# Kernel optimization log

Measured on AMD Instinct MI355X. Metric: run time of the kernel, lower is better.

## Reference

```python
import jax, jax.numpy as jnp
import numpy as np

B, T, H, K, V, O = 4, 2048, 512, 128, 128, 512


def setup_inputs() -> dict:
    key = jax.random.key(0)
    k0, k1, k2 = jax.random.split(key, 3)
    hidden_state = jax.random.normal(k0, (B, T, H), dtype=jnp.float32)
    cell_state = jnp.zeros((B, K, V), dtype=jnp.float32)
    # fused projection: hidden -> [query K, key K, gate K, value V]
    lim_p = np.sqrt(6.0 / (H + 3 * K + V)).astype(np.float32)  # xavier uniform
    proj_w = jax.random.uniform(k1, (3 * K + V, H), jnp.float32, -lim_p, lim_p)
    proj_b = jnp.zeros((3 * K + V,), jnp.float32)
    lim_o = np.sqrt(6.0 / (2 * V + O)).astype(np.float32)
    out_w = jax.random.uniform(k2, (O, 2 * V), jnp.float32, -lim_o, lim_o)
    out_b = jnp.zeros((O,), jnp.float32)
    return {"hidden_state": hidden_state, "cell_state": cell_state,
            "proj_w": proj_w, "proj_b": proj_b, "out_w": out_w, "out_b": out_b}


def reference(hidden_state, cell_state, proj_w, proj_b, out_w, out_b):
    Bq, Tq, _ = hidden_state.shape
    qkgv = hidden_state @ proj_w.T + proj_b          # (B,T,3K+V)
    query = qkgv[..., :K]
    kgate = jax.nn.sigmoid(qkgv[..., K:2 * K])       # key (sigmoid)
    gate = jax.nn.sigmoid(qkgv[..., 2 * K:3 * K])
    value = jnp.tanh(qkgv[..., 3 * K:])              # (B,T,V)

    def step(C, xs):
        q_t, k_t, g_t, v_t = xs                      # (B,K),(B,K),(B,K),(B,V)
        C = C * g_t[..., None] + k_t[..., None] * v_t[..., None, :]  # (B,K,V)
        o_t = jnp.einsum('bkv,bk->bv', C, q_t)       # C^T q
        return C, o_t

    xs = (query.swapaxes(0, 1), kgate.swapaxes(0, 1),
          gate.swapaxes(0, 1), value.swapaxes(0, 1))
    C_final, ov = jax.lax.scan(step, cell_state, xs)
    ov = ov.swapaxes(0, 1)                           # (B,T,V) output_val per step

    # causal Luong dot attention over the growing bank of past output_vals
    scores = jnp.einsum('btv,bsv->bts', ov, ov)      # (B,T,T)
    causal = jnp.tril(jnp.ones((Tq, Tq), dtype=bool))
    scores = jnp.where(causal, scores, -jnp.inf)
    attn = jax.nn.softmax(scores, axis=-1)
    context = jnp.einsum('bts,bsv->btv', attn, ov)   # (B,T,V)

    outputs = jnp.concatenate([ov, context], axis=-1) @ out_w.T + out_b  # (B,T,O)
    return outputs, C_final
```

## Files before the change

kernel.cpp:

```cpp
#include <hip/hip_runtime.h>
#include <hip/hip_bf16.h>


typedef __attribute__((ext_vector_type(8))) short bf16x8;
typedef __attribute__((ext_vector_type(4))) float f32x4;
typedef __attribute__((ext_vector_type(4))) short short4v;

#define MFMA(a,b,c) __builtin_amdgcn_mfma_f32_16x16x32_bf16(a,b,c,0,0,0)

__device__ __forceinline__ short f2b(float x){
  union { float f; unsigned u; } v; v.f = x;
  unsigned r = v.u + 0x7fffu + ((v.u >> 16) & 1u);
  return (short)(r >> 16);
}
__device__ __forceinline__ float b2f(short h){
  union { unsigned u; float f; } v;
  v.u = ((unsigned)(unsigned short)h) << 16;
  return v.f;
}
__device__ __forceinline__ void split2(float x, short& h, short& l){
  h = f2b(x);
  l = f2b(x - b2f(h));
}

__global__ void k_split(const float* __restrict__ in, short* __restrict__ hi,
                        short* __restrict__ lo, int n){
  int i = (blockIdx.x * blockDim.x + threadIdx.x) * 4;
  if (i < n){
    float4 v = *(const float4*)(in + i);
    short4v h, l;
    short th, tl;
    split2(v.x, th, tl); h.x = th; l.x = tl;
    split2(v.y, th, tl); h.y = th; l.y = tl;
    split2(v.z, th, tl); h.z = th; l.z = tl;
    split2(v.w, th, tl); h.w = th; l.w = tl;
    *(short4v*)(hi + i) = h;
    *(short4v*)(lo + i) = l;
  }
}

__global__ void k_cvt(const float* __restrict__ in, short* __restrict__ out, int n){
  int i = (blockIdx.x * blockDim.x + threadIdx.x) * 4;
  if (i < n){
    float4 v = *(const float4*)(in + i);
    short4v o; o.x = f2b(v.x); o.y = f2b(v.y); o.z = f2b(v.z); o.w = f2b(v.w);
    *(short4v*)(out + i) = o;
  }
}

__global__ __launch_bounds__(256) void k_gemm1(
    const short* __restrict__ Ah, const short* __restrict__ Al,
    const short* __restrict__ Bh, const short* __restrict__ Bl,
    const float* __restrict__ bias,
    float* __restrict__ q_o, float* __restrict__ kg_o,
    float* __restrict__ lg_o, float* __restrict__ vv_o)
{
  const int Kd = 512;
  __shared__ __align__(16) short Ash[128][40], Asl[128][40];
  __shared__ __align__(16) short Bsh[64][40],  Bsl[64][40];
  const int m0 = blockIdx.x * 128, n0 = blockIdx.y * 64;
  const int tid = threadIdx.x, lane = tid & 63, w = tid >> 6;
  const int wr = w >> 1, wc = w & 1;
  const int coll = lane & 15, rq = lane >> 4;
  f32x4 acc[4][2];
#pragma unroll
  for (int i = 0; i < 4; i++)
#pragma unroll
    for (int j = 0; j < 2; j++) acc[i][j] = (f32x4){0.f,0.f,0.f,0.f};

  const int ar = tid >> 1, ac = (tid & 1) * 16;
  const int br = tid >> 2, bc = (tid & 3) * 8;

  for (int k0 = 0; k0 < Kd; k0 += 32){
    __syncthreads();
    { size_t g = (size_t)(m0 + ar) * Kd + k0 + ac;
      *(bf16x8*)&Ash[ar][ac]     = *(const bf16x8*)(Ah + g);
      *(bf16x8*)&Ash[ar][ac + 8] = *(const bf16x8*)(Ah + g + 8);
      *(bf16x8*)&Asl[ar][ac]     = *(const bf16x8*)(Al + g);
      *(bf16x8*)&Asl[ar][ac + 8] = *(const bf16x8*)(Al + g + 8); }
    { size_t g = (size_t)(n0 + br) * Kd + k0 + bc;
      *(bf16x8*)&Bsh[br][bc] = *(const bf16x8*)(Bh + g);
      *(bf16x8*)&Bsl[br][bc] = *(const bf16x8*)(Bl + g); }
    __syncthreads();
    bf16x8 ah[4], al[4], bh[2], bl[2];
#pragma unroll
    for (int mi = 0; mi < 4; mi++){
      ah[mi] = *(const bf16x8*)&Ash[wr*64 + mi*16 + coll][rq*8];
      al[mi] = *(const bf16x8*)&Asl[wr*64 + mi*16 + coll][rq*8];
    }
#pragma unroll
    for (int ni = 0; ni < 2; ni++){
      bh[ni] = *(const bf16x8*)&Bsh[wc*32 + ni*16 + coll][rq*8];
      bl[ni] = *(const bf16x8*)&Bsl[wc*32 + ni*16 + coll][rq*8];
    }
#pragma unroll
    for (int mi = 0; mi < 4; mi++)
#pragma unroll
      for (int ni = 0; ni < 2; ni++){
        acc[mi][ni] = MFMA(ah[mi], bh[ni], acc[mi][ni]);
        acc[mi][ni] = MFMA(ah[mi], bl[ni], acc[mi][ni]);
        acc[mi][ni] = MFMA(al[mi], bh[ni], acc[mi][ni]);
      }
  }
#pragma unroll
  for (int mi = 0; mi < 4; mi++)
#pragma unroll
  for (int ni = 0; ni < 2; ni++){
    int gn = n0 + wc*32 + ni*16 + coll;
    float bsv = bias[gn];
    int sec = gn >> 7, jj = gn & 127;
#pragma unroll
    for (int r = 0; r < 4; r++){
      int gm = m0 + wr*64 + mi*16 + rq*4 + r;
      float v = acc[mi][ni][r] + bsv;
      size_t idx = (size_t)gm * 128 + jj;
      if (sec == 0)      q_o[idx] = v;
      else if (sec == 1) kg_o[idx] = 1.f / (1.f + __expf(-v));
      else if (sec == 2) lg_o[idx] = (v > 0.f) ? -log1pf(__expf(-v)) : (v - log1pf(__expf(v)));
      else               vv_o[idx] = tanhf(v);
    }
  }
}

__global__ __launch_bounds__(128) void k_prep(
  const float* __restrict__ q_f, const float* __restrict__ kg_f,
  const float* __restrict__ lg_f, const float* __restrict__ vv_f,
  short* __restrict__ qth, short* __restrict__ qtl,
  short* __restrict__ kth, short* __restrict__ ktl,
  short* __restrict__ khTh, short* __restrict__ khTl,
  short* __restrict__ vvTh, short* __restrict__ vvTl,
  float* __restrict__ Dend)
{
  const int bc = blockIdx.x;
  const int kx = threadIdx.x;
  const size_t base = ((size_t)(bc >> 6) * 2048 + (size_t)(bc & 63) * 32) * 128 + kx;
  double L[32];
  double Lr = 0.0;
#pragma unroll
  for (int s = 0; s < 32; s++){
    size_t idx = base + (size_t)s * 128;
    Lr += (double)lg_f[idx];
    L[s] = Lr;
    float lam  = __expf((float)Lr);
    float ilam = __expf((float)(-Lr));
    short h, l;
    split2(q_f[idx] * lam, h, l);  qth[idx] = h; qtl[idx] = l;
    split2(kg_f[idx] * ilam, h, l); kth[idx] = h; ktl[idx] = l;
  }
  const double Lend = Lr;
  Dend[(size_t)bc * 128 + kx] = (float)exp(Lend);
  __align__(16) short bufh[32], bufl[32];
#pragma unroll
  for (int s = 0; s < 32; s++){
    size_t idx = base + (size_t)s * 128;
    short h, l;
    split2(kg_f[idx] * __expf((float)(Lend - L[s])), h, l);
    bufh[s] = h; bufl[s] = l;
  }
  { short* dh = khTh + ((size_t)bc * 128 + kx) * 32;
    short* dl = khTl + ((size_t)bc * 128 + kx) * 32;
#pragma unroll
    for (int i = 0; i < 32; i += 8){
      *(bf16x8*)(dh + i) = *(const bf16x8*)(bufh + i);
      *(bf16x8*)(dl + i) = *(const bf16x8*)(bufl + i);
    } }
#pragma unroll
  for (int s = 0; s < 32; s++){
    short h, l;
    split2(vv_f[base + (size_t)s * 128], h, l);
    bufh[s] = h; bufl[s] = l;
  }
  { short* dh = vvTh + ((size_t)bc * 128 + kx) * 32;
    short* dl = vvTl + ((size_t)bc * 128 + kx) * 32;
#pragma unroll
    for (int i = 0; i < 32; i += 8){
      *(bf16x8*)(dh + i) = *(const bf16x8*)(bufh + i);
      *(bf16x8*)(dl + i) = *(const bf16x8*)(bufl + i);
    } }
}

__global__ __launch_bounds__(64) void k_scan(
  const short* __restrict__ khTh, const short* __restrict__ khTl,
  const short* __restrict__ vvTh, const short* __restrict__ vvTl,
  const float* __restrict__ Dend, const float* __restrict__ cell0,
  short* __restrict__ sth, short* __restrict__ stl, float* __restrict__ Cfin)
{
  const int blk = blockIdx.x;
  const int b = blk >> 6, tile = blk & 63;
  const int kt = tile >> 3, vt = tile & 7;
  const int lane = threadIdx.x & 63;
  const int coll = lane & 15, rq = lane >> 4;
  const int kcol = kt*16 + coll;
  const int vrow0 = vt*16 + rq*4;
  const size_t cb0 = (size_t)b * 64;

  f32x4 acc;
#pragma unroll
  for (int r = 0; r < 4; r++)
    acc[r] = cell0[((size_t)b*128 + kcol)*128 + vrow0 + r];

  size_t gv = (cb0*128 + vt*16 + coll)*32 + rq*8;
  size_t gk = (cb0*128 + kt*16 + coll)*32 + rq*8;
  bf16x8 avh = *(const bf16x8*)(vvTh + gv);
  bf16x8 avl = *(const bf16x8*)(vvTl + gv);
  bf16x8 bkh = *(const bf16x8*)(khTh + gk);
  bf16x8 bkl = *(const bf16x8*)(khTl + gk);
  float d = Dend[cb0*128 + kcol];

  for (int ck = 0; ck < 64; ck++){
    const size_t cb = cb0 + ck;
    const size_t cbn = cb0 + (ck < 63 ? ck + 1 : ck);
    size_t ngv = (cbn*128 + vt*16 + coll)*32 + rq*8;
    size_t ngk = (cbn*128 + kt*16 + coll)*32 + rq*8;
    bf16x8 navh = *(const bf16x8*)(vvTh + ngv);
    bf16x8 navl = *(const bf16x8*)(vvTl + ngv);
    bf16x8 nbkh = *(const bf16x8*)(khTh + ngk);
    bf16x8 nbkl = *(const bf16x8*)(khTl + ngk);
    float nd = Dend[cbn*128 + kcol];
    {
      size_t sb = (cb*128 + vrow0)*128 + kcol;
#pragma unroll
      for (int r = 0; r < 4; r++){
        short h, l; split2(acc[r], h, l);
        sth[sb + (size_t)r*128] = h;
        stl[sb + (size_t)r*128] = l;
      }
    }
#pragma unroll
    for (int r = 0; r < 4; r++) acc[r] *= d;
    acc = MFMA(avh, bkh, acc);
    acc = MFMA(avh, bkl, acc);
    acc = MFMA(avl, bkh, acc);
    avh = navh; avl = navl; bkh = nbkh; bkl = nbkl; d = nd;
  }
  *(f32x4*)(Cfin + ((size_t)b*128 + kcol)*128 + vrow0) = acc;
}

__global__ __launch_bounds__(256) void k_chunkout(
  const short* __restrict__ qth, const short* __restrict__ qtl,
  const short* __restrict__ kth, const short* __restrict__ ktl,
  const short* __restrict__ vvTh, const short* __restrict__ vvTl,
  const short* __restrict__ sth, const short* __restrict__ stl,
  short* __restrict__ ovT, short* __restrict__ ovc,
  short* __restrict__ ovqh, short* __restrict__ ovql)
{
  __shared__ __align__(16) short ATh[32][40], ATl[32][40];
  const int bc = blockIdx.x;
  const int b = bc >> 6, ck = bc & 63;
  const int tid = threadIdx.x, lane = tid & 63, w = tid >> 6;
  const int coll = lane & 15, rq = lane >> 4;
  const size_t tbase = (size_t)b * 2048 + (size_t)ck * 32;
  {
    const int si = w >> 1, ti = w & 1;
    f32x4 aA = (f32x4){0.f,0.f,0.f,0.f};
#pragma unroll
    for (int kit = 0; kit < 4; kit++){
      size_t ga = (tbase + si*16 + coll) * 128 + kit*32 + rq*8;
      size_t gb = (tbase + ti*16 + coll) * 128 + kit*32 + rq*8;
      bf16x8 a3h = *(const bf16x8*)(kth + ga), a3l = *(const bf16x8*)(ktl + ga);
      bf16x8 b3h = *(const bf16x8*)(qth + gb), b3l = *(const bf16x8*)(qtl + gb);
      aA = MFMA(a3h, b3h, aA);
      aA = MFMA(a3h, b3l, aA);
      aA = MFMA(a3l, b3h, aA);
    }
#pragma unroll
    for (int r = 0; r < 4; r++){
      int s = si*16 + rq*4 + r, t = ti*16 + coll;
      float val = (s <= t) ? aA[r] : 0.f;
      short h, l; split2(val, h, l);
      ATh[t][s] = h; ATl[t][s] = l;
    }
  }
  __syncthreads();
  const int vb = w * 32;
  f32x4 o[2][2];
#pragma unroll
  for (int vi = 0; vi < 2; vi++)
#pragma unroll
    for (int ti = 0; ti < 2; ti++) o[vi][ti] = (f32x4){0.f,0.f,0.f,0.f};
#pragma unroll
  for (int kit = 0; kit < 4; kit++){
    bf16x8 aCh[2], aCl[2], bqh[2], bql[2];
#pragma unroll
    for (int vi = 0; vi < 2; vi++){
      size_t g = ((size_t)bc * 128 + vb + vi*16 + coll) * 128 + kit*32 + rq*8;
      aCh[vi] = *(const bf16x8*)(sth + g);
      aCl[vi] = *(const bf16x8*)(stl + g);
    }
#pragma unroll
    for (int ti = 0; ti < 2; ti++){
      size_t g = (tbase + ti*16 + coll) * 128 + kit*32 + rq*8;
      bqh[ti] = *(const bf16x8*)(qth + g);
      bql[ti] = *(const bf16x8*)(qtl + g);
    }
#pragma unroll
    for (int vi = 0; vi < 2; vi++)
#pragma unroll
      for (int ti = 0; ti < 2; ti++){
        o[vi][ti] = MFMA(aCh[vi], bqh[ti], o[vi][ti]);
        o[vi][ti] = MFMA(aCh[vi], bql[ti], o[vi][ti]);
        o[vi][ti] = MFMA(aCl[vi], bqh[ti], o[vi][ti]);
      }
  }
  {
    bf16x8 a2h[2], a2l[2], b2h[2], b2l[2];
#pragma unroll
    for (int vi = 0; vi < 2; vi++){
      size_t g = ((size_t)bc * 128 + vb + vi*16 + coll) * 32 + rq*8;
      a2h[vi] = *(const bf16x8*)(vvTh + g);
      a2l[vi] = *(const bf16x8*)(vvTl + g);
    }
#pragma unroll
    for (int ti = 0; ti < 2; ti++){
      b2h[ti] = *(const bf16x8*)&ATh[ti*16 + coll][rq*8];
      b2l[ti] = *(const bf16x8*)&ATl[ti*16 + coll][rq*8];
    }
#pragma unroll
    for (int vi = 0; vi < 2; vi++)
#pragma unroll
      for (int ti = 0; ti < 2; ti++){
        o[vi][ti] = MFMA(a2h[vi], b2h[ti], o[vi][ti]);
        o[vi][ti] = MFMA(a2h[vi], b2l[ti], o[vi][ti]);
        o[vi][ti] = MFMA(a2l[vi], b2h[ti], o[vi][ti]);
      }
  }
#pragma unroll
  for (int vi = 0; vi < 2; vi++)
#pragma unroll
  for (int ti = 0; ti < 2; ti++)
#pragma unroll
  for (int r = 0; r < 4; r++){
    int v = vb + vi*16 + rq*4 + r;
    int tl = ti*16 + coll;
    float val = o[vi][ti][r];
    short h, l; split2(val, h, l);
    ovT[((size_t)b * 128 + v) * 2048 + (size_t)ck * 32 + tl] = h;
    ovc[(tbase + tl) * 256 + v] = h;
    ovqh[(tbase + tl) * 128 + v] = h;
    ovql[(tbase + tl) * 128 + v] = l;
  }
}

__global__ __launch_bounds__(256) void k_attn(
  const short* __restrict__ ovqh, const short* __restrict__ ovql,
  const short* __restrict__ ovT, short* __restrict__ ovc)
{
  __shared__ __align__(16) short P[4][16][40];
  const int blk = blockIdx.x;
  const int b = blk >> 5, qi = blk & 31;
  const int qbase = qi * 64;
  const int tid = threadIdx.x, lane = tid & 63, w = tid >> 6;
  const int coll = lane & 15, rq = lane >> 4;
  const int tw = qbase + w * 16;
  const size_t obase = (size_t)b * 2048;
  bf16x8 qfh[4], qfl[4];
#pragma unroll
  for (int kit = 0; kit < 4; kit++){
    size_t g = (obase + tw + coll) * 128 + kit*32 + rq*8;
    qfh[kit] = *(const bf16x8*)(ovqh + g);
    qfl[kit] = *(const bf16x8*)(ovql + g);
  }
  float m[4], l[4];
  f32x4 oa[8];
#pragma unroll
  for (int r = 0; r < 4; r++){ m[r] = -1e30f; l[r] = 0.f; }
#pragma unroll
  for (int df = 0; df < 8; df++) oa[df] = (f32x4){0.f,0.f,0.f,0.f};
  const int smaxv = tw + 15;
  for (int s0 = 0; s0 <= smaxv; s0 += 32){
    f32x4 sc[2];
#pragma unroll
    for (int sf = 0; sf < 2; sf++){
      f32x4 a = (f32x4){0.f,0.f,0.f,0.f};
#pragma unroll
      for (int kit = 0; kit < 4; kit++){
        size_t g = (obase + s0 + sf*16 + coll) * 128 + kit*32 + rq*8;
        bf16x8 kfh = *(const bf16x8*)(ovqh + g);
        bf16x8 kfl = *(const bf16x8*)(ovql + g);
        a = MFMA(qfh[kit], kfh, a);
        a = MFMA(qfh[kit], kfl, a);
        a = MFMA(qfl[kit], kfh, a);
        a = MFMA(qfl[kit], kfl, a);
      }
      sc[sf] = a;
    }
#pragma unroll
    for (int r = 0; r < 4; r++){
      int trow = tw + rq*4 + r;
      float s0v = (s0 + coll      <= trow) ? sc[0][r] : -1e30f;
      float s1v = (s0 + 16 + coll <= trow) ? sc[1][r] : -1e30f;
      float mx = fmaxf(s0v, s1v);
#pragma unroll
      for (int d = 1; d < 16; d <<= 1) mx = fmaxf(mx, __shfl_xor(mx, d));
      float mn = fmaxf(m[r], mx);
      float scale = __expf(m[r] - mn);
      float p0 = __expf(s0v - mn);
      float p1 = __expf(s1v - mn);
      float rs = p0 + p1;
#pragma unroll
      for (int d = 1; d < 16; d <<= 1) rs += __shfl_xor(rs, d);
      l[r] = l[r] * scale + rs;
      m[r] = mn;
#pragma unroll
      for (int df = 0; df < 8; df++) oa[df][r] *= scale;
      P[w][rq*4 + r][coll]      = f2b(p0);
      P[w][rq*4 + r][16 + coll] = f2b(p1);
    }
    bf16x8 pf = *(const bf16x8*)&P[w][coll][rq*8];
#pragma unroll
    for (int df = 0; df < 8; df++){
      bf16x8 vf = *(const bf16x8*)(ovT + ((size_t)b * 128 + df*16 + coll) * 2048 + s0 + rq*8);
      oa[df] = MFMA(pf, vf, oa[df]);
    }
  }
#pragma unroll
  for (int df = 0; df < 8; df++)
#pragma unroll
    for (int r = 0; r < 4; r++){
      int t = tw + rq*4 + r;
      ovc[(obase + t) * 256 + 128 + df*16 + coll] = f2b(oa[df][r] / l[r]);
    }
}

__global__ __launch_bounds__(256) void k_gemm0(
  const short* __restrict__ A, const short* __restrict__ Bw,
  const float* __restrict__ bias, float* __restrict__ out)
{
  const int Kd = 256, N = 512;
  __shared__ __align__(16) short As[128][40];
  __shared__ __align__(16) short Bs[64][40];
  const int m0 = blockIdx.x * 128, n0 = blockIdx.y * 64;
  const int tid = threadIdx.x, lane = tid & 63, w = tid >> 6;
  const int wr = w >> 1, wc = w & 1;
  const int coll = lane & 15, rq = lane >> 4;
  f32x4 acc[4][2];
#pragma unroll
  for (int i = 0; i < 4; i++)
#pragma unroll
    for (int j = 0; j < 2; j++) acc[i][j] = (f32x4){0.f,0.f,0.f,0.f};
  const int ar = tid >> 1, ac = (tid & 1) * 16;
  const int br = tid >> 2, bc = (tid & 3) * 8;
  for (int k0 = 0; k0 < Kd; k0 += 32){
    __syncthreads();
    { const short* g = A + (size_t)(m0 + ar) * Kd + k0 + ac;
      *(bf16x8*)&As[ar][ac]     = *(const bf16x8*)g;
      *(bf16x8*)&As[ar][ac + 8] = *(const bf16x8*)(g + 8); }
    { const short* g = Bw + (size_t)(n0 + br) * Kd + k0 + bc;
      *(bf16x8*)&Bs[br][bc] = *(const bf16x8*)g; }
    __syncthreads();
    bf16x8 a[4], b[2];
#pragma unroll
    for (int mi = 0; mi < 4; mi++) a[mi] = *(const bf16x8*)&As[wr*64 + mi*16 + coll][rq*8];
#pragma unroll
    for (int ni = 0; ni < 2; ni++) b[ni] = *(const bf16x8*)&Bs[wc*32 + ni*16 + coll][rq*8];
#pragma unroll
    for (int mi = 0; mi < 4; mi++)
#pragma unroll
      for (int ni = 0; ni < 2; ni++) acc[mi][ni] = MFMA(a[mi], b[ni], acc[mi][ni]);
  }
#pragma unroll
  for (int mi = 0; mi < 4; mi++)
#pragma unroll
  for (int ni = 0; ni < 2; ni++){
    int gn = n0 + wc*32 + ni*16 + coll;
    float bsv = bias[gn];
#pragma unroll
    for (int r = 0; r < 4; r++){
      int gm = m0 + wr*64 + mi*16 + rq*4 + r;
      out[(size_t)gm * N + gn] = acc[mi][ni][r] + bsv;
    }
  }
}

extern "C" void kernel_launch(void* const* d_in, const int* in_sizes, int n_in,
                              void* d_out, int out_size, void* d_ws, size_t ws_size,
                              hipStream_t stream){
  const float* hidden = (const float*)d_in[0];
  const float* cell0  = (const float*)d_in[1];
  const float* projw  = (const float*)d_in[2];
  const float* projb  = (const float*)d_in[3];
  const float* outw   = (const float*)d_in[4];
  const float* outb   = (const float*)d_in[5];
  float* out = (float*)d_out;

  char* ws = (char*)d_ws;
  size_t off = 0;
  auto alloc = [&](size_t bytes) -> void* {
    void* p = ws + off;
    off += (bytes + 255) & ~(size_t)255;
    return p;
  };
  short* Xh   = (short*)alloc(8192ULL * 512 * 2);
  short* Xl   = (short*)alloc(8192ULL * 512 * 2);
  short* ovqh = Xh;
  short* ovql = Xh + 1048576;
  short* ovT  = Xh + 2097152;
  short* ovc  = Xh + 3145728;
  float* q_f  = (float*)alloc(8192ULL * 128 * 4);
  float* kg_f = (float*)alloc(8192ULL * 128 * 4);
  float* lg_f = (float*)alloc(8192ULL * 128 * 4);
  float* vv_f = (float*)alloc(8192ULL * 128 * 4);
  short* sth  = (short*)q_f;
  short* stl  = sth + 4194304;
  short* Wh   = (short*)alloc(512ULL * 512 * 2);
  short* Wl   = (short*)alloc(512ULL * 512 * 2);
  short* OWbf = (short*)alloc(512ULL * 256 * 2);
  short* qth  = (short*)alloc(8192ULL * 128 * 2);
  short* qtl  = (short*)alloc(8192ULL * 128 * 2);
  short* kth  = (short*)alloc(8192ULL * 128 * 2);
  short* ktl  = (short*)alloc(8192ULL * 128 * 2);
  short* khTh = (short*)alloc(256ULL * 128 * 32 * 2);
  short* khTl = (short*)alloc(256ULL * 128 * 32 * 2);
  short* vvTh = (short*)alloc(256ULL * 128 * 32 * 2);
  short* vvTl = (short*)alloc(256ULL * 128 * 32 * 2);
  float* Dend = (float*)alloc(256ULL * 128 * 4);

  k_split<<<4096, 256, 0, stream>>>(hidden, Xh, Xl, 8192 * 512);
  k_split<<<256,  256, 0, stream>>>(projw,  Wh, Wl, 512 * 512);
  k_cvt<<<128, 256, 0, stream>>>(outw, OWbf, 512 * 256);

  k_gemm1<<<dim3(64, 8), 256, 0, stream>>>(Xh, Xl, Wh, Wl, projb, q_f, kg_f, lg_f, vv_f);
  k_prep<<<256, 128, 0, stream>>>(q_f, kg_f, lg_f, vv_f,
                                  qth, qtl, kth, ktl, khTh, khTl, vvTh, vvTl, Dend);
  k_scan<<<256, 64, 0, stream>>>(khTh, khTl, vvTh, vvTl, Dend, cell0,
                                 sth, stl, out + 8192ULL * 512);
  k_chunkout<<<256, 256, 0, stream>>>(qth, qtl, kth, ktl, vvTh, vvTl, sth, stl,
                                      ovT, ovc, ovqh, ovql);
  k_attn<<<128, 256, 0, stream>>>(ovqh, ovql, ovT, ovc);
  k_gemm0<<<dim3(64, 8), 256, 0, stream>>>(ovc, OWbf, outb, out);
}
```

Before: 364.5 us.

## Split causal attention over key partitions and add a combine kernel

The attention kernel previously ran 128 blocks, each walking all causal keys serially. It now splits the key range into 8 partitions of 256 (grid 32x4x8), so each block emits partial max, sum and bf16 unnormalized outputs, and a new combine kernel merges them with log-sum-exp weighting. It also drops the low*low split-bf16 MFMA term, uses three independent accumulators, and prefetches V fragments before the softmax. The aim is to fill many more CUs on a long serial loop, at the cost of an extra launch, partial-buffer traffic, bf16 rounding of partials and slightly lower score precision.

Result: faster. 293.8 us (-19.4%).

```diff
diff --git a/kernel.cpp b/kernel.cpp
--- a/kernel.cpp
+++ b/kernel.cpp
@@ -343,16 +343,23 @@
 
 __global__ __launch_bounds__(256) void k_attn(
   const short* __restrict__ ovqh, const short* __restrict__ ovql,
-  const short* __restrict__ ovT, short* __restrict__ ovc)
-{
+  const short* __restrict__ ovT,
+  float* __restrict__ m_part, float* __restrict__ l_part,
+  short* __restrict__ oa_part)
+{
+  const int qi = blockIdx.x, b = blockIdx.y, p = blockIdx.z;
+  const int qbase = qi * 64;
+  const int ps = p * 256;
+  const size_t obase = (size_t)b * 2048;
+  const int tid = threadIdx.x;
+  if (ps > qbase + 63){
+    if (tid < 64) l_part[((obase + qbase + tid) << 3) + p] = 0.f;
+    return;
+  }
   __shared__ __align__(16) short P[4][16][40];
-  const int blk = blockIdx.x;
-  const int b = blk >> 5, qi = blk & 31;
-  const int qbase = qi * 64;
-  const int tid = threadIdx.x, lane = tid & 63, w = tid >> 6;
+  const int lane = tid & 63, w = tid >> 6;
   const int coll = lane & 15, rq = lane >> 4;
   const int tw = qbase + w * 16;
-  const size_t obase = (size_t)b * 2048;
   bf16x8 qfh[4], qfl[4];
 #pragma unroll
   for (int kit = 0; kit < 4; kit++){
@@ -366,24 +373,33 @@
   for (int r = 0; r < 4; r++){ m[r] = -1e30f; l[r] = 0.f; }
 #pragma unroll
   for (int df = 0; df < 8; df++) oa[df] = (f32x4){0.f,0.f,0.f,0.f};
-  const int smaxv = tw + 15;
-  for (int s0 = 0; s0 <= smaxv; s0 += 32){
+  const int send = min(tw + 15, ps + 255);
+  for (int s0 = ps; s0 <= send; s0 += 32){
     f32x4 sc[2];
 #pragma unroll
     for (int sf = 0; sf < 2; sf++){
-      f32x4 a = (f32x4){0.f,0.f,0.f,0.f};
+      bf16x8 kh[4], kl[4];
 #pragma unroll
       for (int kit = 0; kit < 4; kit++){
         size_t g = (obase + s0 + sf*16 + coll) * 128 + kit*32 + rq*8;
-        bf16x8 kfh = *(const bf16x8*)(ovqh + g);
-        bf16x8 kfl = *(const bf16x8*)(ovql + g);
-        a = MFMA(qfh[kit], kfh, a);
-        a = MFMA(qfh[kit], kfl, a);
-        a = MFMA(qfl[kit], kfh, a);
-        a = MFMA(qfl[kit], kfl, a);
-      }
-      sc[sf] = a;
-    }
+        kh[kit] = *(const bf16x8*)(ovqh + g);
+        kl[kit] = *(const bf16x8*)(ovql + g);
+      }
+      f32x4 c0 = (f32x4){0.f,0.f,0.f,0.f};
+      f32x4 c1 = (f32x4){0.f,0.f,0.f,0.f};
+      f32x4 c2 = (f32x4){0.f,0.f,0.f,0.f};
+#pragma unroll
+      for (int kit = 0; kit < 4; kit++){
+        c0 = MFMA(qfh[kit], kh[kit], c0);
+        c1 = MFMA(qfh[kit], kl[kit], c1);
+        c2 = MFMA(qfl[kit], kh[kit], c2);
+      }
+      sc[sf] = c0 + c1 + c2;
+    }
+    bf16x8 vf[8];
+#pragma unroll
+    for (int df = 0; df < 8; df++)
+      vf[df] = *(const bf16x8*)(ovT + ((size_t)b*128 + df*16 + coll)*2048 + s0 + rq*8);
 #pragma unroll
     for (int r = 0; r < 4; r++){
       int trow = tw + rq*4 + r;
@@ -408,18 +424,66 @@
     }
     bf16x8 pf = *(const bf16x8*)&P[w][coll][rq*8];
 #pragma unroll
-    for (int df = 0; df < 8; df++){
-      bf16x8 vf = *(const bf16x8*)(ovT + ((size_t)b * 128 + df*16 + coll) * 2048 + s0 + rq*8);
-      oa[df] = MFMA(pf, vf, oa[df]);
-    }
-  }
-#pragma unroll
-  for (int df = 0; df < 8; df++)
-#pragma unroll
-    for (int r = 0; r < 4; r++){
-      int t = tw + rq*4 + r;
-      ovc[(obase + t) * 256 + 128 + df*16 + coll] = f2b(oa[df][r] / l[r]);
-    }
+    for (int df = 0; df < 8; df++)
+      oa[df] = MFMA(pf, vf[df], oa[df]);
+  }
+#pragma unroll
+  for (int r = 0; r < 4; r++){
+    int t = tw + rq*4 + r;
+    size_t idx8 = ((obase + t) << 3) + p;
+    if (coll == 0){ m_part[idx8] = m[r]; l_part[idx8] = l[r]; }
+#pragma unroll
+    for (int df = 0; df < 8; df++)
+      oa_part[idx8*128 + df*16 + coll] = f2b(oa[df][r]);
+  }
+}
+
+__global__ __launch_bounds__(256) void k_comb(
+  const float* __restrict__ m_part, const float* __restrict__ l_part,
+  const short* __restrict__ oa_part, short* __restrict__ ovc)
+{
+  const int blk = blockIdx.x;
+  const int b = blk >> 5, qi = blk & 31;
+  const int row = threadIdx.x >> 2, cg = threadIdx.x & 3;
+  const int t = qi*64 + row;
+  const size_t base8 = ((size_t)b*2048 + t) * 8;
+  float mv[8], lv[8];
+#pragma unroll
+  for (int p = 0; p < 8; p++){ mv[p] = m_part[base8+p]; lv[p] = l_part[base8+p]; }
+  float M = -3e38f;
+#pragma unroll
+  for (int p = 0; p < 8; p++) if (lv[p] > 0.f) M = fmaxf(M, mv[p]);
+  float L = 0.f, wgt[8];
+#pragma unroll
+  for (int p = 0; p < 8; p++){
+    wgt[p] = (lv[p] > 0.f) ? __expf(mv[p] - M) : 0.f;
+    L += lv[p] * wgt[p];
+  }
+  const float inv = 1.f / L;
+  const int v0 = cg * 32;
+  float acc[32];
+#pragma unroll
+  for (int j = 0; j < 32; j++) acc[j] = 0.f;
+#pragma unroll
+  for (int p = 0; p < 8; p++){
+    if (lv[p] > 0.f){
+      const short* src = oa_part + (base8 + p)*128 + v0;
+#pragma unroll
+      for (int jo = 0; jo < 32; jo += 8){
+        bf16x8 x = *(const bf16x8*)(src + jo);
+#pragma unroll
+        for (int j = 0; j < 8; j++) acc[jo+j] += b2f(x[j]) * wgt[p];
+      }
+    }
+  }
+  short* dst = ovc + ((size_t)b*2048 + t)*256 + 128 + v0;
+#pragma unroll
+  for (int jo = 0; jo < 32; jo += 8){
+    bf16x8 o;
+#pragma unroll
+    for (int j = 0; j < 8; j++) o[j] = f2b(acc[jo+j] * inv);
+    *(bf16x8*)(dst + jo) = o;
+  }
 }
 
 __global__ __launch_bounds__(256) void k_gemm0(
@@ -502,6 +566,7 @@
   float* vv_f = (float*)alloc(8192ULL * 128 * 4);
   short* sth  = (short*)q_f;
   short* stl  = sth + 4194304;
+  short* oa_part = (short*)q_f;
   short* Wh   = (short*)alloc(512ULL * 512 * 2);
   short* Wl   = (short*)alloc(512ULL * 512 * 2);
   short* OWbf = (short*)alloc(512ULL * 256 * 2);
@@ -514,6 +579,8 @@
   short* vvTh = (short*)alloc(256ULL * 128 * 32 * 2);
   short* vvTl = (short*)alloc(256ULL * 128 * 32 * 2);
   float* Dend = (float*)alloc(256ULL * 128 * 4);
+  float* m_part = (float*)alloc(4ULL * 2048 * 8 * 4);
+  float* l_part = (float*)alloc(4ULL * 2048 * 8 * 4);
 
   k_split<<<4096, 256, 0, stream>>>(hidden, Xh, Xl, 8192 * 512);
   k_split<<<256,  256, 0, stream>>>(projw,  Wh, Wl, 512 * 512);
@@ -526,6 +593,7 @@
                                  sth, stl, out + 8192ULL * 512);
   k_chunkout<<<256, 256, 0, stream>>>(qth, qtl, kth, ktl, vvTh, vvTl, sth, stl,
                                       ovT, ovc, ovqh, ovql);
-  k_attn<<<128, 256, 0, stream>>>(ovqh, ovql, ovT, ovc);
+  k_attn<<<dim3(32, 4, 8), 256, 0, stream>>>(ovqh, ovql, ovT, m_part, l_part, oa_part);
+  k_comb<<<128, 256, 0, stream>>>(m_part, l_part, oa_part, ovc);
   k_gemm0<<<dim3(64, 8), 256, 0, stream>>>(ovc, OWbf, outb, out);
 }
```
